# Optimization experiments

Hardware: AMD Instinct MI355X
Metric: run time of the kernel (lower is better)

## Reference

```python
import jax, jax.numpy as jnp
import numpy as np

B, N, F, H = 2, 2048, 1024, 16
D = F // H  # head_dim = 64
SCALE = D ** -0.5


def setup_inputs() -> dict:
    key = jax.random.key(0)
    ks = jax.random.split(key, 5)
    std = F ** -0.5
    return {
        "x": jax.random.normal(ks[0], (B, N, F), dtype=jnp.float32),
        "Wq": jax.random.normal(ks[1], (F, F), dtype=jnp.float32) * std,
        "Wk": jax.random.normal(ks[2], (F, F), dtype=jnp.float32) * std,
        "Wv": jax.random.normal(ks[3], (F, F), dtype=jnp.float32) * std,
        "Wo": jax.random.normal(ks[4], (F, F), dtype=jnp.float32) * std,
        "bo": jnp.zeros((F,), dtype=jnp.float32),
    }


def reference(x, Wq, Wk, Wv, Wo, bo):
    b, n, f = x.shape
    # nn.Linear computes x @ W.T
    q = (x @ Wq.T).reshape(b, n, H, D).transpose(0, 2, 1, 3)  # bhnd
    k = (x @ Wk.T).reshape(b, n, H, D).transpose(0, 2, 1, 3)
    v = (x @ Wv.T).reshape(b, n, H, D).transpose(0, 2, 1, 3)
    score = jax.nn.softmax(jnp.einsum('bhif,bhjf->bhij', q, k) * SCALE, axis=-1)
    attn = jnp.einsum('bhij,bhjf->bihf', score, v)  # (b, n, h, d)
    o = attn.reshape(b, n, f) @ Wo.T + bo
    return o
```

## Files before the change

kernel.cpp:

```cpp
#include <hip/hip_runtime.h>
#include <hip/hip_bf16.h>

#define B_    2
#define NSEQ  2048
#define FDIM  1024
#define NH    16
#define HD    64
#define MTOT  (B_*NSEQ)
#define BHSZ  (NSEQ*HD)

typedef __bf16 bf16_t;
typedef __bf16 bf16x4 __attribute__((ext_vector_type(4)));
typedef __bf16 bf16x8 __attribute__((ext_vector_type(8)));
typedef float  f32x4  __attribute__((ext_vector_type(4)));

#define AS1 __attribute__((address_space(1)))
#define AS3 __attribute__((address_space(3)))

__device__ __forceinline__ void gld_lds16(const bf16_t* g, bf16_t* l) {
  __builtin_amdgcn_global_load_lds((const AS1 void*)g, (AS3 void*)l, 16, 0, 0);
}

__device__ __forceinline__ f32x4 mfma_pv(bf16x4 a, bf16x4 b, f32x4 c) {
#if defined(__HIP_DEVICE_COMPILE__)
#if __has_builtin(__builtin_amdgcn_mfma_f32_16x16x16bf16_1k)
  typedef short s4 __attribute__((ext_vector_type(4)));
  return __builtin_amdgcn_mfma_f32_16x16x16bf16_1k(
      __builtin_bit_cast(s4, a), __builtin_bit_cast(s4, b), c, 0, 0, 0);
#else
  asm("v_mfma_f32_16x16x16_bf16 %0, %1, %2, %0" : "+v"(c) : "v"(a), "v"(b));
  return c;
#endif
#else
  (void)a; (void)b;
  return c;
#endif
}

extern "C" __global__ __launch_bounds__(256) void cast_all_k(
    const float* __restrict__ x,  const float* __restrict__ wq,
    const float* __restrict__ wk, const float* __restrict__ wv,
    const float* __restrict__ wo,
    bf16_t* __restrict__ xb,  bf16_t* __restrict__ wqb,
    bf16_t* __restrict__ wkb, bf16_t* __restrict__ wvb,
    bf16_t* __restrict__ wob)
{
  long t = (long)blockIdx.x * blockDim.x + threadIdx.x;
  long i = t * 4;
  const float* src; bf16_t* dst; long off;
  if      (i < 4194304L) { src = x;  dst = xb;  off = i; }
  else if (i < 5242880L) { src = wq; dst = wqb; off = i - 4194304L; }
  else if (i < 6291456L) { src = wk; dst = wkb; off = i - 5242880L; }
  else if (i < 7340032L) { src = wv; dst = wvb; off = i - 6291456L; }
  else                   { src = wo; dst = wob; off = i - 7340032L; }
  float4 v = *(const float4*)(src + off);
  bf16x4 o = { (bf16_t)v.x, (bf16_t)v.y, (bf16_t)v.z, (bf16_t)v.w };
  *(bf16x4*)(dst + off) = o;
}

extern "C" __global__ __launch_bounds__(512) void gemm_bt_k(
    const bf16_t* __restrict__ A,
    const bf16_t* __restrict__ Bq, const bf16_t* __restrict__ Bk,
    const bf16_t* __restrict__ Bv,
    bf16_t* __restrict__ oq, bf16_t* __restrict__ okk,
    bf16_t* __restrict__ ovt)
{
  __shared__ __align__(16) char garena[33792];
  bf16_t* As = (bf16_t*)garena;
  bf16_t* Bs = (bf16_t*)(garena + 16384);
  const int K = FDIM;
  int mode = blockIdx.z;
  const bf16_t* Bw = (mode == 0) ? Bq : (mode == 1) ? Bk : Bv;
  int m0 = blockIdx.x * 128, n0 = blockIdx.y * 128;
  int tid = threadIdx.x, lane = tid & 63, wave = tid >> 6;
  int g = lane >> 4, c = lane & 15;
  int wm = (wave & 1) * 64, wn = (wave >> 1) * 32;
  f32x4 acc[4][2];
  for (int i = 0; i < 4; ++i)
    for (int j = 0; j < 2; ++j)
      acc[i][j] = (f32x4){0.f, 0.f, 0.f, 0.f};

  int srow = lane >> 2;
  int scol = (lane & 3) * 8;

  for (int kt = 0; kt < K / 64; ++kt) {
    int kk = kt * 64;
    {
      int chunk = wave;
      const bf16_t* ag = A  + (long)(m0 + chunk*16 + srow) * K + kk + scol;
      const bf16_t* bg = Bw + (long)(n0 + chunk*16 + srow) * K + kk + scol;
      gld_lds16(ag,      As + chunk * 512);
      gld_lds16(ag + 32, As + 4096 + chunk * 512);
      gld_lds16(bg,      Bs + chunk * 512);
      gld_lds16(bg + 32, Bs + 4096 + chunk * 512);
    }
    __syncthreads();
    bf16x8 af[4][2], bfr[2][2];
    for (int t = 0; t < 4; ++t) {
      af[t][0]  = *(const bf16x8*)(As + (wm + t*16 + c) * 32 + g * 8);
      af[t][1]  = *(const bf16x8*)(As + 4096 + (wm + t*16 + c) * 32 + g * 8);
    }
    for (int t = 0; t < 2; ++t) {
      bfr[t][0] = *(const bf16x8*)(Bs + (wn + t*16 + c) * 32 + g * 8);
      bfr[t][1] = *(const bf16x8*)(Bs + 4096 + (wn + t*16 + c) * 32 + g * 8);
    }
    for (int mt = 0; mt < 4; ++mt)
      for (int nt = 0; nt < 2; ++nt) {
        acc[mt][nt] = __builtin_amdgcn_mfma_f32_16x16x32_bf16(
            af[mt][0], bfr[nt][0], acc[mt][nt], 0, 0, 0);
        acc[mt][nt] = __builtin_amdgcn_mfma_f32_16x16x32_bf16(
            af[mt][1], bfr[nt][1], acc[mt][nt], 0, 0, 0);
      }
    __syncthreads();
  }

  bf16_t* Tl = (bf16_t*)garena;
  float sc = (mode == 0) ? 0.125f : 1.0f;
  if (mode < 2) {
    for (int mt = 0; mt < 4; ++mt)
      for (int nt = 0; nt < 2; ++nt) {
        int nloc = wn + nt*16 + c;
        for (int r = 0; r < 4; ++r) {
          int mloc = wm + mt*16 + g*4 + r;
          Tl[mloc*132 + nloc] = (bf16_t)(acc[mt][nt][r] * sc);
        }
      }
  } else {
    for (int mt = 0; mt < 4; ++mt)
      for (int nt = 0; nt < 2; ++nt) {
        int nloc = wn + nt*16 + c;
        int mloc = wm + mt*16 + g*4;
        bf16x4 pk = { (bf16_t)acc[mt][nt][0], (bf16_t)acc[mt][nt][1],
                      (bf16_t)acc[mt][nt][2], (bf16_t)acc[mt][nt][3] };
        *(bf16x4*)(Tl + nloc*132 + mloc) = pk;
      }
  }
  __syncthreads();

  int b = m0 >> 11, m0loc = m0 & 2047;
  int h0 = n0 >> 6, tile0 = m0loc >> 6;
#pragma unroll
  for (int u = 0; u < 4; ++u) {
    int chunk = u * 512 + tid;
    bf16_t* dst;
    int sidx;
    if (mode == 0) {
      int headloc = chunk >> 10, o = chunk & 1023;
      int tokloc = o >> 3, dd = (o & 7) * 8;
      sidx = tokloc*132 + headloc*64 + dd;
      dst = oq + ((long)(b*NH + h0 + headloc) * NSEQ + m0loc) * HD + (long)o * 8;
    } else if (mode == 1) {
      int region = chunk >> 9, o = chunk & 511;
      int headloc = region >> 1, t = region & 1;
      int f = o >> 6, rest = o & 63;
      int mtA = f >> 1, kh = f & 1, gK = rest >> 4, cA = rest & 15;
      int tokloc = t*64 + mtA*16 + cA;
      sidx = tokloc*132 + headloc*64 + kh*32 + gK*8;
      dst = okk + (long)(b*NH + h0 + headloc) * BHSZ
            + (long)(tile0 + t) * 4096 + (long)o * 8;
    } else {
      int region = chunk >> 9, o = chunk & 511;
      int headloc = region >> 1, t = region & 1;
      int frag = o >> 5, so = o & 31;
      int mtA = frag >> 2, dtA = frag & 3;
      int slot0 = so * 2;
      int cA = slot0 >> 2, gA0 = slot0 & 3;
      int k0loc = t*64 + mtA*16 + gA0*4;
      int nloc = headloc*64 + dtA*16 + cA;
      sidx = nloc*132 + k0loc;
      dst = ovt + (long)(b*NH + h0 + headloc) * BHSZ
            + (long)(tile0 + t) * 4096 + (long)o * 8;
    }
    bf16x4 lo = *(const bf16x4*)(Tl + sidx);
    bf16x4 hi = *(const bf16x4*)(Tl + sidx + 4);
    bf16x8 v;
#pragma unroll
    for (int i = 0; i < 4; ++i) { v[i] = lo[i]; v[i+4] = hi[i]; }
    *(bf16x8*)dst = v;
  }
}

extern "C" __global__ __launch_bounds__(512) void gemm_out_k(
    const bf16_t* __restrict__ A, const bf16_t* __restrict__ W,
    const float* __restrict__ bias, float* __restrict__ out)
{
  __shared__ __align__(16) bf16_t As[8192];
  __shared__ __align__(16) bf16_t Bs[4096];
  const int K = FDIM;
  int m0 = blockIdx.x * 128, n0 = blockIdx.y * 64;
  int tid = threadIdx.x, lane = tid & 63, wave = tid >> 6;
  int g = lane >> 4, c = lane & 15;
  int wm = (wave & 3) * 32, wn = (wave >> 2) * 32;
  f32x4 acc[2][2];
  for (int i = 0; i < 2; ++i)
    for (int j = 0; j < 2; ++j)
      acc[i][j] = (f32x4){0.f, 0.f, 0.f, 0.f};

  int srow = lane >> 2;
  int scol = (lane & 3) * 8;

  for (int kt = 0; kt < K / 64; ++kt) {
    int kk = kt * 64;
    {
      const bf16_t* ag = A + (long)(m0 + wave*16 + srow) * K + kk + scol;
      gld_lds16(ag,      As + wave * 512);
      gld_lds16(ag + 32, As + 4096 + wave * 512);
      if (wave < 4) {
        const bf16_t* bg = W + (long)(n0 + wave*16 + srow) * K + kk + scol;
        gld_lds16(bg,      Bs + wave * 512);
        gld_lds16(bg + 32, Bs + 2048 + wave * 512);
      }
    }
    __syncthreads();
    bf16x8 af[2][2], bfr[2][2];
    for (int t = 0; t < 2; ++t) {
      af[t][0]  = *(const bf16x8*)(As + (wm + t*16 + c) * 32 + g * 8);
      af[t][1]  = *(const bf16x8*)(As + 4096 + (wm + t*16 + c) * 32 + g * 8);
      bfr[t][0] = *(const bf16x8*)(Bs + (wn + t*16 + c) * 32 + g * 8);
      bfr[t][1] = *(const bf16x8*)(Bs + 2048 + (wn + t*16 + c) * 32 + g * 8);
    }
    for (int mt = 0; mt < 2; ++mt)
      for (int nt = 0; nt < 2; ++nt) {
        acc[mt][nt] = __builtin_amdgcn_mfma_f32_16x16x32_bf16(
            af[mt][0], bfr[nt][0], acc[mt][nt], 0, 0, 0);
        acc[mt][nt] = __builtin_amdgcn_mfma_f32_16x16x32_bf16(
            af[mt][1], bfr[nt][1], acc[mt][nt], 0, 0, 0);
      }
    __syncthreads();
  }

  for (int mt = 0; mt < 2; ++mt)
    for (int nt = 0; nt < 2; ++nt) {
      int n = n0 + wn + nt*16 + c;
      float bv = bias[n];
      for (int r = 0; r < 4; ++r) {
        int m = m0 + wm + mt*16 + g*4 + r;
        out[(long)m * FDIM + n] = acc[mt][nt][r] + bv;
      }
    }
}

extern "C" __global__ __launch_bounds__(512) void attn_fused_k(
    const bf16_t* __restrict__ q, const bf16_t* __restrict__ k,
    const bf16_t* __restrict__ vt, bf16_t* __restrict__ attn)
{
  __shared__ __align__(16) char arena[65536];
  __shared__ float Ll[128];
  int bh = blockIdx.y;
  int tid = threadIdx.x, lane = tid & 63, wave = tid >> 6;
  int g = lane >> 4, c = lane & 15;
  int qg = wave & 3, half = wave >> 2;
  int qw = blockIdx.x * 128 + qg * 32;
  const bf16_t* Q  = q  + (long)bh * NSEQ * HD;
  const bf16_t* Kf = k  + (long)bh * BHSZ;
  const bf16_t* Vf = vt + (long)bh * BHSZ;

  bf16x8 bQ[2][2];
#pragma unroll
  for (int s = 0; s < 2; ++s)
#pragma unroll
    for (int hh = 0; hh < 2; ++hh)
      bQ[s][hh] = *(const bf16x8*)(Q + (long)(qw + s*16 + c) * HD + hh*32 + g*8);

  f32x4 acc[2][4];
  f32x4 lsum[2];
#pragma unroll
  for (int s = 0; s < 2; ++s) {
#pragma unroll
    for (int dt = 0; dt < 4; ++dt) acc[s][dt] = (f32x4){0.f, 0.f, 0.f, 0.f};
    lsum[s] = (f32x4){0.f, 0.f, 0.f, 0.f};
  }

  int w4 = wave & 3, ln = lane;
  const int NT = NSEQ / 128;
  int kbase = half * (NSEQ / 2);

  auto stage = [&](int buf, int k0) {
    bf16_t* Kb = (bf16_t*)(arena + buf * 32768 + half * 16384);
    bf16_t* Vb = Kb + 4096;
    long tbase = (long)(k0 >> 6) * 4096;
#pragma unroll
    for (int j = 0; j < 2; ++j) {
      int ch = j*4 + w4;
      gld_lds16(Kf + tbase + ch*512 + ln*8, Kb + ch*512);
      gld_lds16(Vf + tbase + ch*512 + ln*8, Vb + ch*512);
    }
  };

  stage(0, kbase);
  __syncthreads();

  for (int kt = 0; kt < NT; ++kt) {
    int cur = kt & 1;
    if (kt + 1 < NT) stage(cur ^ 1, kbase + (kt + 1) * 64);

    const bf16_t* Kb = (const bf16_t*)(arena + cur * 32768 + half * 16384);
    const bf16_t* Vb = Kb + 4096;

    f32x4 St[2][4];
#pragma unroll
    for (int mt = 0; mt < 4; ++mt) {
      bf16x8 k0f = *(const bf16x8*)(Kb + (mt*2 + 0) * 512 + lane * 8);
      bf16x8 k1f = *(const bf16x8*)(Kb + (mt*2 + 1) * 512 + lane * 8);
#pragma unroll
      for (int s = 0; s < 2; ++s) {
        f32x4 z = (f32x4){0.f, 0.f, 0.f, 0.f};
        z = __builtin_amdgcn_mfma_f32_16x16x32_bf16(k0f, bQ[s][0], z, 0, 0, 0);
        z = __builtin_amdgcn_mfma_f32_16x16x32_bf16(k1f, bQ[s][1], z, 0, 0, 0);
        St[s][mt] = z;
      }
    }

    bf16x4 bP[2][4];
#pragma unroll
    for (int s = 0; s < 2; ++s)
#pragma unroll
      for (int mt = 0; mt < 4; ++mt) {
#pragma unroll
        for (int r = 0; r < 4; ++r) {
          float p = __expf(St[s][mt][r]);
          St[s][mt][r] = p;
          lsum[s][r] += p;
        }
        bP[s][mt] = (bf16x4){(bf16_t)St[s][mt][0], (bf16_t)St[s][mt][1],
                             (bf16_t)St[s][mt][2], (bf16_t)St[s][mt][3]};
      }

#pragma unroll
    for (int mt = 0; mt < 4; ++mt)
#pragma unroll
      for (int dt = 0; dt < 4; ++dt) {
        bf16x4 aV = *(const bf16x4*)(Vb + (mt*4 + dt) * 256 + (c*4 + g) * 4);
        acc[0][dt] = mfma_pv(aV, bP[0][mt], acc[0][dt]);
        acc[1][dt] = mfma_pv(aV, bP[1][mt], acc[1][dt]);
      }

    __syncthreads();
  }

  float lp[2];
#pragma unroll
  for (int s = 0; s < 2; ++s) {
    float p = (lsum[s][0] + lsum[s][1]) + (lsum[s][2] + lsum[s][3]);
    p += __shfl_xor(p, 16);
    p += __shfl_xor(p, 32);
    lp[s] = p;
  }

  float* Opart = (float*)arena;
  bf16_t* Tb = (bf16_t*)(arena + 36864);
  if (half == 1) {
#pragma unroll
    for (int s = 0; s < 2; ++s) {
      int qrow = qg*32 + s*16 + c;
#pragma unroll
      for (int dt = 0; dt < 4; ++dt)
        *(f32x4*)(Opart + qrow*72 + dt*16 + g*4) = acc[s][dt];
      if (g == 0) Ll[qrow] = lp[s];
    }
  }
  __syncthreads();
  if (half == 0) {
#pragma unroll
    for (int s = 0; s < 2; ++s) {
      int qrow = qg*32 + s*16 + c;
      float inv = 1.f / (lp[s] + Ll[qrow]);
#pragma unroll
      for (int dt = 0; dt < 4; ++dt) {
        f32x4 part = *(const f32x4*)(Opart + qrow*72 + dt*16 + g*4);
#pragma unroll
        for (int r = 0; r < 4; ++r)
          Tb[qrow*80 + dt*16 + g*4 + r] =
              (bf16_t)((acc[s][dt][r] + part[r]) * inv);
      }
    }
  }
  __syncthreads();
  int b = bh >> 4, h = bh & 15;
  int row = tid >> 2, dseg = (tid & 3) * 16;
  const bf16_t* src = Tb + row*80 + dseg;
  bf16_t* dst = attn + ((long)(b * NSEQ + blockIdx.x*128 + row)) * FDIM + h * HD + dseg;
  *(bf16x8*)(dst)     = *(const bf16x8*)(src);
  *(bf16x8*)(dst + 8) = *(const bf16x8*)(src + 8);
}

extern "C" void kernel_launch(void* const* d_in, const int* in_sizes, int n_in,
                              void* d_out, int out_size, void* d_ws, size_t ws_size,
                              hipStream_t stream)
{
  const float* x  = (const float*)d_in[0];
  const float* wq = (const float*)d_in[1];
  const float* wk = (const float*)d_in[2];
  const float* wv = (const float*)d_in[3];
  const float* wo = (const float*)d_in[4];
  const float* bo = (const float*)d_in[5];
  float* out = (float*)d_out;
  char* ws = (char*)d_ws;

  const size_t MB = 1024 * 1024;
  bf16_t* xb    = (bf16_t*)(ws);
  bf16_t* wqb   = (bf16_t*)(ws + 8  * MB);
  bf16_t* wkb   = (bf16_t*)(ws + 10 * MB);
  bf16_t* wvb   = (bf16_t*)(ws + 12 * MB);
  bf16_t* wob   = (bf16_t*)(ws + 14 * MB);
  bf16_t* q_ws  = (bf16_t*)(ws + 16 * MB);
  bf16_t* k_ws  = (bf16_t*)(ws + 24 * MB);
  bf16_t* vt_ws = (bf16_t*)(ws + 32 * MB);
  bf16_t* at_ws = (bf16_t*)(ws + 40 * MB);

  hipLaunchKernelGGL(cast_all_k, dim3(8192), dim3(256), 0, stream,
                     x, wq, wk, wv, wo, xb, wqb, wkb, wvb, wob);

  hipLaunchKernelGGL(gemm_bt_k, dim3(32, 8, 3), dim3(512), 0, stream,
                     xb, wqb, wkb, wvb, q_ws, k_ws, vt_ws);

  hipLaunchKernelGGL(attn_fused_k, dim3(16, 32), dim3(512), 0, stream,
                     q_ws, k_ws, vt_ws, at_ws);

  hipLaunchKernelGGL(gemm_out_k, dim3(32, 16), dim3(512), 0, stream,
                     at_ws, wob, bo, out);
}
```

Baseline: 186.5 us.

## Use 16x16x32 MFMA for PV with repacked V layout and exp2 softmax

Replaces the 16x16x16 bf16 MFMA in the P·V product with the wider 16x16x32 instruction. This halves the number of PV MFMAs and loads V fragments as 8-wide vectors. The V-transpose store layout is reworked to match the new fragment ordering, and the lo/hi halves are read with a mode-dependent offset. The Q scale folds in log2(e) so the softmax can use a hardware exp2 instead of __expf. The risk is layout correctness: the K-index pairing between P and V must match across both MFMA operands.

```diff
diff --git a/kernel.cpp b/kernel.cpp
--- a/kernel.cpp
+++ b/kernel.cpp
@@ -17,24 +17,14 @@
 #define AS1 __attribute__((address_space(1)))
 #define AS3 __attribute__((address_space(3)))
 
+#if __has_builtin(__builtin_amdgcn_exp2f)
+#define EXP2(x) __builtin_amdgcn_exp2f(x)
+#else
+#define EXP2(x) exp2f(x)
+#endif
+
 __device__ __forceinline__ void gld_lds16(const bf16_t* g, bf16_t* l) {
   __builtin_amdgcn_global_load_lds((const AS1 void*)g, (AS3 void*)l, 16, 0, 0);
-}
-
-__device__ __forceinline__ f32x4 mfma_pv(bf16x4 a, bf16x4 b, f32x4 c) {
-#if defined(__HIP_DEVICE_COMPILE__)
-#if __has_builtin(__builtin_amdgcn_mfma_f32_16x16x16bf16_1k)
-  typedef short s4 __attribute__((ext_vector_type(4)));
-  return __builtin_amdgcn_mfma_f32_16x16x16bf16_1k(
-      __builtin_bit_cast(s4, a), __builtin_bit_cast(s4, b), c, 0, 0, 0);
-#else
-  asm("v_mfma_f32_16x16x16_bf16 %0, %1, %2, %0" : "+v"(c) : "v"(a), "v"(b));
-  return c;
-#endif
-#else
-  (void)a; (void)b;
-  return c;
-#endif
 }
 
 extern "C" __global__ __launch_bounds__(256) void cast_all_k(
@@ -115,7 +105,7 @@
   }
 
   bf16_t* Tl = (bf16_t*)garena;
-  float sc = (mode == 0) ? 0.125f : 1.0f;
+  float sc = (mode == 0) ? 0.18033688011112042f : 1.0f;
   if (mode < 2) {
     for (int mt = 0; mt < 4; ++mt)
       for (int nt = 0; nt < 2; ++nt) {
@@ -139,6 +129,7 @@
 
   int b = m0 >> 11, m0loc = m0 & 2047;
   int h0 = n0 >> 6, tile0 = m0loc >> 6;
+  int hoff = (mode == 2) ? 16 : 4;
 #pragma unroll
   for (int u = 0; u < 4; ++u) {
     int chunk = u * 512 + tid;
@@ -161,18 +152,14 @@
     } else {
       int region = chunk >> 9, o = chunk & 511;
       int headloc = region >> 1, t = region & 1;
-      int frag = o >> 5, so = o & 31;
-      int mtA = frag >> 2, dtA = frag & 3;
-      int slot0 = so * 2;
-      int cA = slot0 >> 2, gA0 = slot0 & 3;
-      int k0loc = t*64 + mtA*16 + gA0*4;
-      int nloc = headloc*64 + dtA*16 + cA;
-      sidx = nloc*132 + k0loc;
+      int c2 = o >> 8, dt = (o >> 6) & 3, ln = o & 63;
+      int gA = ln >> 4, cA = ln & 15;
+      sidx = (headloc*64 + dt*16 + cA) * 132 + t*64 + c2*32 + gA*4;
       dst = ovt + (long)(b*NH + h0 + headloc) * BHSZ
             + (long)(tile0 + t) * 4096 + (long)o * 8;
     }
     bf16x4 lo = *(const bf16x4*)(Tl + sidx);
-    bf16x4 hi = *(const bf16x4*)(Tl + sidx + 4);
+    bf16x4 hi = *(const bf16x4*)(Tl + sidx + hoff);
     bf16x8 v;
 #pragma unroll
     for (int i = 0; i < 4; ++i) { v[i] = lo[i]; v[i+4] = hi[i]; }
@@ -311,28 +298,34 @@
       }
     }
 
-    bf16x4 bP[2][4];
+    bf16x8 bP[2][2];
 #pragma unroll
     for (int s = 0; s < 2; ++s)
 #pragma unroll
-      for (int mt = 0; mt < 4; ++mt) {
+      for (int c2 = 0; c2 < 2; ++c2) {
+        f32x4 pa = St[s][c2*2 + 0];
+        f32x4 pb = St[s][c2*2 + 1];
+        bf16x8 t;
 #pragma unroll
         for (int r = 0; r < 4; ++r) {
-          float p = __expf(St[s][mt][r]);
-          St[s][mt][r] = p;
-          lsum[s][r] += p;
+          float x0 = EXP2(pa[r]);
+          float x1 = EXP2(pb[r]);
+          lsum[s][r] += x0 + x1;
+          t[r]     = (bf16_t)x0;
+          t[r + 4] = (bf16_t)x1;
         }
-        bP[s][mt] = (bf16x4){(bf16_t)St[s][mt][0], (bf16_t)St[s][mt][1],
-                             (bf16_t)St[s][mt][2], (bf16_t)St[s][mt][3]};
-      }
-
-#pragma unroll
-    for (int mt = 0; mt < 4; ++mt)
+        bP[s][c2] = t;
+      }
+
+#pragma unroll
+    for (int c2 = 0; c2 < 2; ++c2)
 #pragma unroll
       for (int dt = 0; dt < 4; ++dt) {
-        bf16x4 aV = *(const bf16x4*)(Vb + (mt*4 + dt) * 256 + (c*4 + g) * 4);
-        acc[0][dt] = mfma_pv(aV, bP[0][mt], acc[0][dt]);
-        acc[1][dt] = mfma_pv(aV, bP[1][mt], acc[1][dt]);
+        bf16x8 aV = *(const bf16x8*)(Vb + (c2*4 + dt) * 512 + lane * 8);
+        acc[0][dt] = __builtin_amdgcn_mfma_f32_16x16x32_bf16(
+            aV, bP[0][c2], acc[0][dt], 0, 0, 0);
+        acc[1][dt] = __builtin_amdgcn_mfma_f32_16x16x32_bf16(
+            aV, bP[1][c2], acc[1][dt], 0, 0, 0);
       }
 
     __syncthreads();
```

Result: faster. 174.5 us (-6.4%).
